# Kernel tuning notes

Measured on AMD Instinct MI355X. Metric: run time of the kernel, lower is better.

Reference implementation:

```python
import jax, jax.numpy as jnp
import numpy as np
import math

N_BITS = 8
NUM_GROUPS = 32
NUM_HEADS = 8
EPS = 1e-5


def fake_quant(x):
    # UniformAffineQuantizer: dynamic per-tensor asymmetric 8-bit fake quant
    levels = 2 ** N_BITS - 1
    xmin = jnp.minimum(x.min(), 0.0)
    xmax = jnp.maximum(x.max(), 0.0)
    scale = jnp.maximum((xmax - xmin) / levels, 1e-8)
    zp = jnp.round(-xmin / scale)
    xq = jnp.clip(jnp.round(x / scale) + zp, 0, levels)
    return (xq - zp) * scale


def group_norm(x, w, b):
    # x: (B, C, T)
    B, C, T = x.shape
    xg = x.reshape(B, NUM_GROUPS, C // NUM_GROUPS, T)
    mean = xg.mean(axis=(2, 3), keepdims=True)
    var = xg.var(axis=(2, 3), keepdims=True)
    xg = (xg - mean) * jax.lax.rsqrt(var + EPS)
    return xg.reshape(B, C, T) * w[None, :, None] + b[None, :, None]


def setup_inputs() -> dict:
    key = jax.random.key(0)
    ks = jax.random.split(key, 7)
    C = 512
    x = jax.random.normal(ks[0], (8, C, 32, 32), dtype=jnp.float32)
    gn_w = jnp.ones((C,), jnp.float32)
    gn_b = jnp.zeros((C,), jnp.float32)
    qkv_w = jax.random.normal(ks[1], (3 * C, C), jnp.float32) * (1.0 / math.sqrt(C))
    qkv_b = jax.random.normal(ks[2], (3 * C,), jnp.float32) * 0.01
    proj_w = jax.random.normal(ks[3], (C, C), jnp.float32) * (1.0 / math.sqrt(C))
    proj_b = jax.random.normal(ks[4], (C,), jnp.float32) * 0.01
    return {"x": x, "gn_w": gn_w, "gn_b": gn_b, "qkv_w": qkv_w,
            "qkv_b": qkv_b, "proj_w": proj_w, "proj_b": proj_b}


def reference(x, gn_w, gn_b, qkv_w, qkv_b, proj_w, proj_b):
    b, c, *spatial = x.shape
    T = int(np.prod(spatial))
    xf = x.reshape(b, c, T)                       # (B, C, T)
    h = group_norm(xf, gn_w, gn_b)
    qkv = jnp.einsum('oc,bct->bot', qkv_w, h) + qkv_b[None, :, None]  # (B, 3C, T)
    qkv = qkv.reshape(b * NUM_HEADS, -1, T)       # (B*H, 3*ch, T)
    ch = qkv.shape[1] // 3
    q, k, v = jnp.split(qkv, 3, axis=1)
    q = fake_quant(q)
    k = fake_quant(k)
    v = fake_quant(v)
    scale = 1.0 / math.sqrt(math.sqrt(ch))
    w = jnp.einsum('bct,bcs->bts', q * scale, k * scale)
    w = jax.nn.softmax(w.astype(jnp.float32), axis=-1).astype(q.dtype)
    a = jnp.einsum('bts,bcs->bct', w, v)          # (B*H, ch, T)
    a = a.reshape(b, c, T)
    a = jnp.einsum('oc,bct->bot', proj_w, a) + proj_b[None, :, None]
    return (xf + a).reshape(b, c, *spatial)
```

## Files before the change

kernel.cpp:

```cpp
#include <hip/hip_runtime.h>

typedef __attribute__((ext_vector_type(8))) __bf16 bf16x8;
typedef __attribute__((ext_vector_type(4))) __bf16 bf16x4;
typedef __attribute__((ext_vector_type(4))) float  f32x4;


static constexpr size_t QKV_OFF = 0;
static constexpr size_t HT_OFF  = 50331648;
static constexpr size_t WQ_OFF  = HT_OFF + 8388608;
static constexpr size_t WP_OFF  = WQ_OFF + 1572864;
static constexpr size_t MM_OFF  = WP_OFF + 524288;
static constexpr size_t KI_OFF  = MM_OFF + 8192;
static constexpr size_t VI_OFF  = KI_OFF + 8388608;
static constexpr size_t NEED_NEW = VI_OFF + 8388608;

__device__ __forceinline__ float dqi(float x, float inv_s, float zp) {
    float y = rintf(x * inv_s);
    return fminf(fmaxf(y, -zp), 255.0f - zp);
}
__device__ __forceinline__ f32x4 mfma16(bf16x8 a, bf16x8 b, f32x4 c) {
    return __builtin_amdgcn_mfma_f32_16x16x32_bf16(a, b, c, 0, 0, 0);
}
__device__ __forceinline__ float exp2i(float x) {
    float r;
    asm("v_exp_f32 %0, %1" : "=v"(r) : "v"(x));
    return r;
}
__device__ __forceinline__ void glds16(const __bf16* g, __bf16* l) {
    __builtin_amdgcn_global_load_lds((const __attribute__((address_space(1))) void*)g,
                                     (__attribute__((address_space(3))) void*)l, 16, 0, 0);
}
template <int N> __device__ __forceinline__ void waitv() {
    asm volatile("s_waitcnt vmcnt(%0)" :: "n"(N) : "memory");
}
__device__ __forceinline__ void bar_raw() {
    asm volatile("s_barrier" ::: "memory");
}

__device__ __forceinline__ void red_mm(const float* __restrict__ pmm, int id, int tid,
                                       float* sred, float& mn_out, float& mx_out) {
    float mn = pmm[id * 512 + tid * 2];
    float mx = pmm[id * 512 + tid * 2 + 1];
#pragma unroll
    for (int m = 1; m < 64; m <<= 1) {
        mn = fminf(mn, __shfl_xor(mn, m));
        mx = fmaxf(mx, __shfl_xor(mx, m));
    }
    if ((tid & 63) == 0) { sred[(tid >> 6) * 2] = mn; sred[(tid >> 6) * 2 + 1] = mx; }
    __syncthreads();
    mn = fminf(fminf(sred[0], sred[2]), fminf(sred[4], sred[6]));
    mx = fmaxf(fmaxf(sred[1], sred[3]), fmaxf(sred[5], sred[7]));
    __syncthreads();
    mn_out = fminf(mn, 0.0f);
    mx_out = fmaxf(mx, 0.0f);
}

__device__ __forceinline__ void red_mm8(const float* __restrict__ pmm, int id, int tid,
                                        float* sred, float& mn_out, float& mx_out) {
    int slot = tid & 255;
    float mn = pmm[id * 512 + slot * 2];
    float mx = pmm[id * 512 + slot * 2 + 1];
#pragma unroll
    for (int m = 1; m < 64; m <<= 1) {
        mn = fminf(mn, __shfl_xor(mn, m));
        mx = fmaxf(mx, __shfl_xor(mx, m));
    }
    if ((tid & 63) == 0) { sred[(tid >> 6) * 2] = mn; sred[(tid >> 6) * 2 + 1] = mx; }
    __syncthreads();
    float a = fminf(fminf(sred[0], sred[2]), fminf(sred[4], sred[6]));
    float b = fminf(fminf(sred[8], sred[10]), fminf(sred[12], sred[14]));
    mn = fminf(a, b);
    a = fmaxf(fmaxf(sred[1], sred[3]), fmaxf(sred[5], sred[7]));
    b = fmaxf(fmaxf(sred[9], sred[11]), fmaxf(sred[13], sred[15]));
    mx = fmaxf(a, b);
    __syncthreads();
    mn_out = fminf(mn, 0.0f);
    mx_out = fmaxf(mx, 0.0f);
}

__global__ __launch_bounds__(256) void gnprep(const float* __restrict__ x,
                                              const float* __restrict__ w,
                                              const float* __restrict__ bv,
                                              __bf16* __restrict__ hT,
                                              const float* __restrict__ qw,
                                              __bf16* __restrict__ wq,
                                              const float* __restrict__ pw,
                                              __bf16* __restrict__ wp) {
    int bid = blockIdx.x, tid = threadIdx.x;
    if (bid < 1024) {
        if (bid < 768) {
            int i = bid * 256 + tid;
            float4 v = ((const float4*)qw)[i];
            bf16x4 o = {(__bf16)v.x, (__bf16)v.y, (__bf16)v.z, (__bf16)v.w};
            ((bf16x4*)wq)[i] = o;
        } else {
            int i = (bid - 768) * 256 + tid;
            float4 v = ((const float4*)pw)[i];
            bf16x4 o = {(__bf16)v.x, (__bf16)v.y, (__bf16)v.z, (__bf16)v.w};
            ((bf16x4*)wp)[i] = o;
        }
        return;
    }
    int blk = bid - 1024;
    int b = blk >> 5, g = blk & 31;
    const float* xp = x + (size_t)(b * 512 + g * 16) * 1024;

    float4 v[16];
    float sum = 0.f, ss = 0.f;
#pragma unroll
    for (int i = 0; i < 16; ++i) {
        v[i] = *(const float4*)(xp + (size_t)i * 1024 + tid * 4);
        sum += v[i].x + v[i].y + v[i].z + v[i].w;
        ss  += v[i].x * v[i].x + v[i].y * v[i].y + v[i].z * v[i].z + v[i].w * v[i].w;
    }
#pragma unroll
    for (int m = 1; m < 64; m <<= 1) {
        sum += __shfl_xor(sum, m);
        ss  += __shfl_xor(ss, m);
    }
    __shared__ float s1[4], s2[4];
    int wid = tid >> 6;
    if ((tid & 63) == 0) { s1[wid] = sum; s2[wid] = ss; }
    __syncthreads();
    sum = s1[0] + s1[1] + s1[2] + s1[3];
    ss  = s2[0] + s2[1] + s2[2] + s2[3];
    float mean = sum * (1.0f / 16384.0f);
    float var  = ss * (1.0f / 16384.0f) - mean * mean;
    float rstd = rsqrtf(var + 1e-5f);

    float wc[16], bc[16];
#pragma unroll
    for (int c = 0; c < 16; ++c) { wc[c] = w[g * 16 + c] * rstd; bc[c] = bv[g * 16 + c]; }

#pragma unroll
    for (int j = 0; j < 4; ++j) {
        int t = tid * 4 + j;
        bf16x8 o0, o1;
#pragma unroll
        for (int c = 0; c < 8; ++c)
            o0[c] = (__bf16)(((&v[c].x)[j] - mean) * wc[c] + bc[c]);
#pragma unroll
        for (int c = 0; c < 8; ++c)
            o1[c] = (__bf16)(((&v[c + 8].x)[j] - mean) * wc[c + 8] + bc[c + 8]);
        __bf16* hp = hT + ((size_t)b * 1024 + t) * 512 + g * 16;
        *(bf16x8*)hp = o0;
        *(bf16x8*)(hp + 8) = o1;
    }
}

template <int MTILE, int MOT, bool MINMAX, bool RESID>
__global__ __launch_bounds__(256, 2) void mgemm5(const __bf16* __restrict__ A,
                                                 const __bf16* __restrict__ Bt,
                                                 const float* __restrict__ bias,
                                                 const float* __restrict__ resid,
                                                 float* __restrict__ out,
                                                 int M, float* __restrict__ pmm) {
    constexpr int NF  = (MTILE == 128) ? 4 : 2;
    constexpr int ASZ = MTILE * 64;
    constexpr int BSZ = 128 * 64;
    constexpr int LA  = MTILE / 32;
    constexpr int L   = LA + 4;
    constexpr int STG = 2 * (ASZ + BSZ) * 2;
    constexpr int CSB = 64 * 132 * 4;
    __shared__ __attribute__((aligned(16))) char smem_raw[(STG > CSB) ? STG : CSB];
    __bf16* sA0 = (__bf16*)smem_raw;
    __bf16* sA1 = sA0 + ASZ;
    __bf16* sB0 = sA1 + ASZ;
    __bf16* sB1 = sB0 + BSZ;
    __shared__ float smn[4], smx[4];

    int tid = threadIdx.x;
    int l = tid & 63, w = tid >> 6;
    int lo = l & 15, hi = l >> 4;

    int f = blockIdx.x;
    constexpr int NWG = MOT * 64;
    int wg = (f & 7) * (NWG / 8) + (f >> 3);
    int mo = wg % MOT, nb = wg / MOT;
    int nt = nb & 7, b = nb >> 3;

    const __bf16* Ap = A + (size_t)mo * MTILE * 512;
    const __bf16* Bp = Bt + ((size_t)b * 1024 + (size_t)nt * 128) * 512;
    int m0 = (MTILE == 128) ? (w >> 1) * 64 : 0;
    int n0 = (MTILE == 128) ? (w & 1) * 64 : w * 32;
    f32x4 acc[4][NF] = {};
    int scd = tid & 7;

    auto STAGE = [&](__bf16* dA, __bf16* dB, int k0) {
#pragma unroll
        for (int p = 0; p < LA; ++p) {
            int lin = p * 2048 + tid * 8;
            int row = lin >> 6;
            glds16(Ap + (size_t)row * 512 + k0 + ((scd ^ (row & 7)) << 3), dA + lin);
        }
#pragma unroll
        for (int p = 0; p < 4; ++p) {
            int lin = p * 2048 + tid * 8;
            int row = lin >> 6;
            glds16(Bp + (size_t)row * 512 + k0 + ((scd ^ (row & 7)) << 3), dB + lin);
        }
    };
    auto COMPUTE = [&](const __bf16* cA, const __bf16* cB) {
#pragma unroll
        for (int kk = 0; kk < 2; ++kk) {
            int rch = ((kk * 4 + hi) ^ (lo & 7)) << 3;
            bf16x8 af[4], bfr[NF];
#pragma unroll
            for (int i = 0; i < 4; ++i) af[i] = *(const bf16x8*)&cA[(m0 + 16 * i + lo) * 64 + rch];
#pragma unroll
            for (int j = 0; j < NF; ++j) bfr[j] = *(const bf16x8*)&cB[(n0 + 16 * j + lo) * 64 + rch];
#pragma unroll
            for (int i = 0; i < 4; ++i)
#pragma unroll
                for (int j = 0; j < NF; ++j) acc[i][j] = mfma16(af[i], bfr[j], acc[i][j]);
        }
    };

    STAGE(sA0, sB0, 0);
#pragma unroll
    for (int kp = 0; kp < 8; kp += 2) {
        if (kp + 1 < 8) { STAGE(sA1, sB1, (kp + 1) * 64); waitv<L>(); } else { waitv<0>(); }
        bar_raw();
        COMPUTE(sA0, sB0);
        bar_raw();
        if (kp + 2 < 8) { STAGE(sA0, sB0, (kp + 2) * 64); waitv<L>(); } else { waitv<0>(); }
        bar_raw();
        COMPUTE(sA1, sB1);
        bar_raw();
    }

    float* cs = (float*)smem_raw;
    float mn = 1e30f, mx = -1e30f;
    constexpr int NH = (MTILE == 128) ? 2 : 1;
#pragma unroll
    for (int h = 0; h < NH; ++h) {
        __syncthreads();
        if (MTILE == 64 || (w >> 1) == h) {
#pragma unroll
            for (int i = 0; i < 4; ++i)
#pragma unroll
                for (int r = 0; r < 4; ++r) {
                    int rl = 16 * i + hi * 4 + r;
                    float bi = bias[mo * MTILE + h * 64 + rl];
#pragma unroll
                    for (int j = 0; j < NF; ++j)
                        cs[rl * 132 + n0 + 16 * j + lo] = acc[i][j][r] + bi;
                }
        }
        __syncthreads();
#pragma unroll
        for (int it = 0; it < 8; ++it) {
            int lin = it * 256 + tid;
            int rr = lin >> 5, cc = (lin & 31) << 2;
            float4 v = *(const float4*)&cs[rr * 132 + cc];
            if (MINMAX) {
                mn = fminf(mn, fminf(fminf(v.x, v.y), fminf(v.z, v.w)));
                mx = fmaxf(mx, fmaxf(fmaxf(v.x, v.y), fmaxf(v.z, v.w)));
            }
            int grow = mo * MTILE + h * 64 + rr;
            size_t gaddr = ((size_t)b * M + grow) * 1024 + nt * 128 + cc;
            if (RESID) {
                float4 rv = *(const float4*)&resid[gaddr];
                v.x += rv.x; v.y += rv.y; v.z += rv.z; v.w += rv.w;
            }
            *(float4*)&out[gaddr] = v;
        }
    }

    if (MINMAX) {
#pragma unroll
        for (int msk = 1; msk < 64; msk <<= 1) {
            mn = fminf(mn, __shfl_xor(mn, msk));
            mx = fmaxf(mx, __shfl_xor(mx, msk));
        }
        if (l == 0) { smn[w] = mn; smx[w] = mx; }
        __syncthreads();
        if (tid == 0) {
            mn = fminf(fminf(smn[0], smn[1]), fminf(smn[2], smn[3]));
            mx = fmaxf(fmaxf(smx[0], smx[1]), fmaxf(smx[2], smx[3]));
            int id = mo >> 2;
            int slot = nb * 4 + (mo & 3);
            pmm[id * 512 + slot * 2]     = mn;
            pmm[id * 512 + slot * 2 + 1] = mx;
        }
    }
}

__global__ __launch_bounds__(256) void quant_kv(const float* __restrict__ qkv,
                                                const float* __restrict__ pmm,
                                                __bf16* __restrict__ ki,
                                                __bf16* __restrict__ vi) {
    int bh = blockIdx.x, tt = blockIdx.y;
    int b = bh >> 3, hh = bh & 7;
    int t0 = tt * 64;
    const float* kg = qkv + ((size_t)(b * 1536 + hh * 192) + 64) * 1024;
    const float* vg = kg + 65536;
    int tid = threadIdx.x;

    __shared__ float sred[8];
    float mn1, mx1, mn2, mx2;
    red_mm(pmm, 1, tid, sred, mn1, mx1);
    red_mm(pmm, 2, tid, sred, mn2, mx2);
    float ksc = fmaxf((mx1 - mn1) * (1.f / 255.f), 1e-8f), kzp = rintf(-mn1 / ksc);
    float vsc = fmaxf((mx2 - mn2) * (1.f / 255.f), 1e-8f), vzp = rintf(-mn2 / vsc);
    float inv_k = 1.f / ksc, inv_v = 1.f / vsc;

    __shared__ __bf16 sT[64][68];
    int cr = tid >> 4, t4 = tid & 15;
    int s = tid >> 2, c0 = (tid & 3) * 16;

    __bf16* vd = vi + (size_t)bh * 65536;
#pragma unroll
    for (int r = 0; r < 4; ++r) {
        int c = 16 * r + cr;
        float4 v = *(const float4*)(vg + (size_t)c * 1024 + t0 + t4 * 4);
        bf16x4 o = {(__bf16)dqi(v.x, inv_v, vzp), (__bf16)dqi(v.y, inv_v, vzp),
                    (__bf16)dqi(v.z, inv_v, vzp), (__bf16)dqi(v.w, inv_v, vzp)};
        *(bf16x4*)(vd + (size_t)c * 1024 + t0 + t4 * 4) = o;
    }

#pragma unroll
    for (int r = 0; r < 4; ++r) {
        int c = 16 * r + cr;
        float4 v = *(const float4*)(kg + (size_t)c * 1024 + t0 + t4 * 4);
        sT[t4 * 4 + 0][c] = (__bf16)dqi(v.x, inv_k, kzp);
        sT[t4 * 4 + 1][c] = (__bf16)dqi(v.y, inv_k, kzp);
        sT[t4 * 4 + 2][c] = (__bf16)dqi(v.z, inv_k, kzp);
        sT[t4 * 4 + 3][c] = (__bf16)dqi(v.w, inv_k, kzp);
    }
    __syncthreads();
    bf16x8 a0 = *(const bf16x8*)&sT[s][c0];
    bf16x8 a1 = *(const bf16x8*)&sT[s][c0 + 8];
    __bf16* kd = ki + ((size_t)bh * 1024 + t0 + s) * 64 + c0;
    *(bf16x8*)kd = a0;
    *(bf16x8*)(kd + 8) = a1;
}

__global__ __launch_bounds__(512, 4) void attn5(const float* __restrict__ qkv,
                                                const __bf16* __restrict__ ki,
                                                const __bf16* __restrict__ vi,
                                                const float* __restrict__ pmm,
                                                __bf16* __restrict__ aT) {
    int f = blockIdx.x;
    int bh = (f & 7) * 8 + ((f >> 3) & 7);
    int tt = f >> 6;
    int b = bh >> 3, hh = bh & 7;
    int t0 = tt * 128;
    const float* qg = qkv + (size_t)(b * 1536 + hh * 192) * 1024;
    const __bf16* kb = ki + (size_t)bh * 65536;
    const __bf16* vb = vi + (size_t)bh * 65536;
    int tid = threadIdx.x;

    __shared__ float sred[16];
    float mn0, mx0, mn1, mx1, mn2, mx2;
    red_mm8(pmm, 0, tid, sred, mn0, mx0);
    red_mm8(pmm, 1, tid, sred, mn1, mx1);
    red_mm8(pmm, 2, tid, sred, mn2, mx2);
    float qsc = fmaxf((mx0 - mn0) * (1.f / 255.f), 1e-8f), qzp = rintf(-mn0 / qsc);
    float ksc = fmaxf((mx1 - mn1) * (1.f / 255.f), 1e-8f);
    float vsc = fmaxf((mx2 - mn2) * (1.f / 255.f), 1e-8f);
    float inv_q = 1.f / qsc;
    float alpha2 = qsc * ksc * 0.125f * 1.4426950408889634f;
    float thr = 11.5415603f / alpha2;

    __shared__ __bf16 sh[128][72];
    __shared__ __bf16 kS[2][4096];
    __shared__ __bf16 vS[2][4096];
    int l = tid & 63, w = tid >> 6;
    int lo = l & 15, hi = l >> 4;

    int srow = tid >> 3, sc = tid & 7;
    int swz = (sc ^ (srow & 7)) << 3;
    const __bf16* kROW = kb + (size_t)srow * 64;
    const __bf16* vROW = vb + (size_t)srow * 1024;
    int lx = lo & 7;
    int rc0 = (hi ^ lx) << 3;
    int rc1 = ((4 + hi) ^ lx) << 3;

    bf16x8 kr = *(const bf16x8*)(kROW + sc * 8);
    bf16x8 vr = *(const bf16x8*)(vROW + sc * 8);

    {
        int c0 = (tid >> 5) * 4;
        int tl = tid & 31;
#pragma unroll
        for (int r = 0; r < 4; ++r) {
            int t = tl + 32 * r;
            float y0 = dqi(qg[(size_t)(c0 + 0) * 1024 + t0 + t], inv_q, qzp);
            float y1 = dqi(qg[(size_t)(c0 + 1) * 1024 + t0 + t], inv_q, qzp);
            float y2 = dqi(qg[(size_t)(c0 + 2) * 1024 + t0 + t], inv_q, qzp);
            float y3 = dqi(qg[(size_t)(c0 + 3) * 1024 + t0 + t], inv_q, qzp);
            bf16x4 o = {(__bf16)y0, (__bf16)y1, (__bf16)y2, (__bf16)y3};
            *(bf16x4*)&sh[t][c0] = o;
        }
    }
    __syncthreads();
    bf16x8 qf0 = *(const bf16x8*)&sh[16 * w + lo][hi * 8];
    bf16x8 qf1 = *(const bf16x8*)&sh[16 * w + lo][32 + hi * 8];
    *(bf16x8*)(kS[0] + srow * 64 + swz) = kr;
    *(bf16x8*)(vS[0] + srow * 64 + swz) = vr;
    __syncthreads();

    f32x4 acc0 = {}, acc1 = {}, acc2 = {}, acc3 = {};
    float m_run = -1e30f, l_run = 0.f;

    for (int st = 0; st < 16; ++st) {
        const __bf16* kc = kS[st & 1];
        const __bf16* vc = vS[st & 1];
        if (st < 15) {
            kr = *(const bf16x8*)(kROW + (st + 1) * 4096 + sc * 8);
            vr = *(const bf16x8*)(vROW + (st + 1) * 64 + sc * 8);
        }

        f32x4 sf[4] = {};
        __builtin_amdgcn_s_setprio(1);
#pragma unroll
        for (int sm = 0; sm < 4; ++sm)
            sf[sm] = mfma16(*(const bf16x8*)(kc + (16 * sm + lo) * 64 + rc0), qf0, sf[sm]);
#pragma unroll
        for (int sm = 0; sm < 4; ++sm)
            sf[sm] = mfma16(*(const bf16x8*)(kc + (16 * sm + lo) * 64 + rc1), qf1, sf[sm]);
        __builtin_amdgcn_s_setprio(0);

        float tm = -1e30f;
#pragma unroll
        for (int sm = 0; sm < 4; ++sm) {
            float a = fmaxf(sf[sm][0], sf[sm][1]);
            float c = fmaxf(sf[sm][2], sf[sm][3]);
            tm = fmaxf(tm, fmaxf(a, c));
        }
        tm = fmaxf(tm, __shfl_xor(tm, 16));
        tm = fmaxf(tm, __shfl_xor(tm, 32));
        if (!__all(tm <= m_run + thr)) {
            float mnew = fmaxf(m_run, tm);
            float fr = exp2i(alpha2 * (m_run - mnew));
            acc0 *= fr; acc1 *= fr; acc2 *= fr; acc3 *= fr;
            l_run *= fr;
            m_run = mnew;
        }
        float cc = -alpha2 * m_run;
        float ts = 0.f;
#pragma unroll
        for (int sm = 0; sm < 4; ++sm)
#pragma unroll
            for (int r = 0; r < 4; ++r) {
                float p = exp2i(fmaf(sf[sm][r], alpha2, cc));
                sf[sm][r] = p;
                ts += p;
            }
        ts += __shfl_xor(ts, 16);
        ts += __shfl_xor(ts, 32);
        l_run += ts;

#pragma unroll
        for (int sm = 0; sm < 4; ++sm) {
            bf16x4 pb = {(__bf16)sf[sm][0], (__bf16)sf[sm][1], (__bf16)sf[sm][2], (__bf16)sf[sm][3]};
            *(bf16x4*)&sh[16 * w + lo][16 * sm + hi * 4] = pb;
        }
        bf16x8 pf0 = *(const bf16x8*)&sh[16 * w + lo][hi * 8];
        bf16x8 pf1 = *(const bf16x8*)&sh[16 * w + lo][32 + hi * 8];

        __builtin_amdgcn_s_setprio(1);
        acc0 = mfma16(*(const bf16x8*)(vc + (lo) * 64 + rc0), pf0, acc0);
        acc1 = mfma16(*(const bf16x8*)(vc + (16 + lo) * 64 + rc0), pf0, acc1);
        acc2 = mfma16(*(const bf16x8*)(vc + (32 + lo) * 64 + rc0), pf0, acc2);
        acc3 = mfma16(*(const bf16x8*)(vc + (48 + lo) * 64 + rc0), pf0, acc3);
        acc0 = mfma16(*(const bf16x8*)(vc + (lo) * 64 + rc1), pf1, acc0);
        acc1 = mfma16(*(const bf16x8*)(vc + (16 + lo) * 64 + rc1), pf1, acc1);
        acc2 = mfma16(*(const bf16x8*)(vc + (32 + lo) * 64 + rc1), pf1, acc2);
        acc3 = mfma16(*(const bf16x8*)(vc + (48 + lo) * 64 + rc1), pf1, acc3);
        __builtin_amdgcn_s_setprio(0);

        if (st < 15) {
            *(bf16x8*)(kS[(st + 1) & 1] + srow * 64 + swz) = kr;
            *(bf16x8*)(vS[(st + 1) & 1] + srow * 64 + swz) = vr;
        }
        __syncthreads();
    }

    float rl = vsc / l_run;
    {
        bf16x4 o0 = {(__bf16)(acc0[0] * rl), (__bf16)(acc0[1] * rl), (__bf16)(acc0[2] * rl), (__bf16)(acc0[3] * rl)};
        bf16x4 o1 = {(__bf16)(acc1[0] * rl), (__bf16)(acc1[1] * rl), (__bf16)(acc1[2] * rl), (__bf16)(acc1[3] * rl)};
        bf16x4 o2 = {(__bf16)(acc2[0] * rl), (__bf16)(acc2[1] * rl), (__bf16)(acc2[2] * rl), (__bf16)(acc2[3] * rl)};
        bf16x4 o3 = {(__bf16)(acc3[0] * rl), (__bf16)(acc3[1] * rl), (__bf16)(acc3[2] * rl), (__bf16)(acc3[3] * rl)};
        *(bf16x4*)&sh[16 * w + lo][0  + hi * 4] = o0;
        *(bf16x4*)&sh[16 * w + lo][16 + hi * 4] = o1;
        *(bf16x4*)&sh[16 * w + lo][32 + hi * 4] = o2;
        *(bf16x4*)&sh[16 * w + lo][48 + hi * 4] = o3;
    }
    __syncthreads();
    __bf16* ap = aT + ((size_t)b * 1024 + t0 + (tid >> 2)) * 512 + hh * 64;
    bf16x8 v0 = *(const bf16x8*)&sh[tid >> 2][(tid & 3) * 8];
    bf16x8 v1 = *(const bf16x8*)&sh[tid >> 2][32 + (tid & 3) * 8];
    *(bf16x8*)(ap + (tid & 3) * 8) = v0;
    *(bf16x8*)(ap + 32 + (tid & 3) * 8) = v1;
}

__global__ __launch_bounds__(256) void attn_mfma(const float* __restrict__ qkv,
                                                 const float* __restrict__ pmm,
                                                 __bf16* __restrict__ aT) {
    int f = blockIdx.x;
    int bh = (f & 7) * 8 + ((f >> 3) & 7);
    int tt = f >> 6;
    int b = bh >> 3, hh = bh & 7;
    int t0 = tt * 64;
    const float* qg = qkv + (size_t)(b * 1536 + hh * 192) * 1024;
    const float* kg = qg + (size_t)64 * 1024;
    const float* vg = qg + (size_t)128 * 1024;
    int tid = threadIdx.x;

    __shared__ float sred[8];
    float mn0, mx0, mn1, mx1, mn2, mx2;
    red_mm(pmm, 0, tid, sred, mn0, mx0);
    red_mm(pmm, 1, tid, sred, mn1, mx1);
    red_mm(pmm, 2, tid, sred, mn2, mx2);
    float qsc = fmaxf((mx0 - mn0) * (1.f / 255.f), 1e-8f), qzp = rintf(-mn0 / qsc);
    float ksc = fmaxf((mx1 - mn1) * (1.f / 255.f), 1e-8f), kzp = rintf(-mn1 / ksc);
    float vsc = fmaxf((mx2 - mn2) * (1.f / 255.f), 1e-8f), vzp = rintf(-mn2 / vsc);
    float inv_q = 1.f / qsc, inv_k = 1.f / ksc, inv_v = 1.f / vsc;
    float alpha = qsc * ksc * 0.125f;

    __shared__ __bf16 qT[64][72];
    __shared__ __bf16 kT[64][72];
    __shared__ __bf16 vL[64][72];
    __shared__ __bf16 pL[4][16][72];

    int l = tid & 63, w = tid >> 6;
    int lo = l & 15, hi = l >> 4;
    int c0 = (tid >> 4) * 4;
    int tl = tid & 15;

#pragma unroll
    for (int r = 0; r < 4; ++r) {
        int t = tl + 16 * r;
        float y0 = dqi(qg[(size_t)(c0 + 0) * 1024 + t0 + t], inv_q, qzp);
        float y1 = dqi(qg[(size_t)(c0 + 1) * 1024 + t0 + t], inv_q, qzp);
        float y2 = dqi(qg[(size_t)(c0 + 2) * 1024 + t0 + t], inv_q, qzp);
        float y3 = dqi(qg[(size_t)(c0 + 3) * 1024 + t0 + t], inv_q, qzp);
        bf16x4 o = {(__bf16)y0, (__bf16)y1, (__bf16)y2, (__bf16)y3};
        *(bf16x4*)&qT[t][c0] = o;
    }
    __syncthreads();
    bf16x8 qf0 = *(const bf16x8*)&qT[16 * w + lo][hi * 8];
    bf16x8 qf1 = *(const bf16x8*)&qT[16 * w + lo][32 + hi * 8];

    f32x4 acc0 = {}, acc1 = {}, acc2 = {}, acc3 = {};
    float m_run = -1e30f, l_run = 0.f;

    for (int st = 0; st < 16; ++st) {
        int s0 = st * 64;
        __syncthreads();
#pragma unroll
        for (int r = 0; r < 4; ++r) {
            int srow = tl + 16 * r;
            float y0 = dqi(kg[(size_t)(c0 + 0) * 1024 + s0 + srow], inv_k, kzp);
            float y1 = dqi(kg[(size_t)(c0 + 1) * 1024 + s0 + srow], inv_k, kzp);
            float y2 = dqi(kg[(size_t)(c0 + 2) * 1024 + s0 + srow], inv_k, kzp);
            float y3 = dqi(kg[(size_t)(c0 + 3) * 1024 + s0 + srow], inv_k, kzp);
            bf16x4 ok = {(__bf16)y0, (__bf16)y1, (__bf16)y2, (__bf16)y3};
            *(bf16x4*)&kT[srow][c0] = ok;
            int c = (tid >> 4) + 16 * r;
            float4 vv = *(const float4*)(vg + (size_t)c * 1024 + s0 + (tid & 15) * 4);
            bf16x4 ov = {(__bf16)dqi(vv.x, inv_v, vzp), (__bf16)dqi(vv.y, inv_v, vzp),
                         (__bf16)dqi(vv.z, inv_v, vzp), (__bf16)dqi(vv.w, inv_v, vzp)};
            *(bf16x4*)&vL[c][(tid & 15) * 4] = ov;
        }
        __syncthreads();

        f32x4 sf[4] = {};
#pragma unroll
        for (int sm = 0; sm < 4; ++sm)
            sf[sm] = mfma16(*(const bf16x8*)&kT[16 * sm + lo][hi * 8], qf0, sf[sm]);
#pragma unroll
        for (int sm = 0; sm < 4; ++sm)
            sf[sm] = mfma16(*(const bf16x8*)&kT[16 * sm + lo][32 + hi * 8], qf1, sf[sm]);

        float tm = -1e30f;
#pragma unroll
        for (int sm = 0; sm < 4; ++sm)
#pragma unroll
            for (int r = 0; r < 4; ++r) { sf[sm][r] *= alpha; tm = fmaxf(tm, sf[sm][r]); }
        tm = fmaxf(tm, __shfl_xor(tm, 16));
        tm = fmaxf(tm, __shfl_xor(tm, 32));
        float mnew = fmaxf(m_run, tm);
        float ts = 0.f;
#pragma unroll
        for (int sm = 0; sm < 4; ++sm)
#pragma unroll
            for (int r = 0; r < 4; ++r) {
                float p = __expf(sf[sm][r] - mnew);
                sf[sm][r] = p;
                ts += p;
            }
        ts += __shfl_xor(ts, 16);
        ts += __shfl_xor(ts, 32);
        float fr = __expf(m_run - mnew);
        l_run = l_run * fr + ts;
        m_run = mnew;
        acc0 *= fr; acc1 *= fr; acc2 *= fr; acc3 *= fr;

#pragma unroll
        for (int sm = 0; sm < 4; ++sm) {
            bf16x4 pb = {(__bf16)sf[sm][0], (__bf16)sf[sm][1], (__bf16)sf[sm][2], (__bf16)sf[sm][3]};
            *(bf16x4*)&pL[w][lo][16 * sm + hi * 4] = pb;
        }
        bf16x8 pf0 = *(const bf16x8*)&pL[w][lo][hi * 8];
        bf16x8 pf1 = *(const bf16x8*)&pL[w][lo][32 + hi * 8];
        acc0 = mfma16(*(const bf16x8*)&vL[lo][hi * 8], pf0, acc0);
        acc1 = mfma16(*(const bf16x8*)&vL[16 + lo][hi * 8], pf0, acc1);
        acc2 = mfma16(*(const bf16x8*)&vL[32 + lo][hi * 8], pf0, acc2);
        acc3 = mfma16(*(const bf16x8*)&vL[48 + lo][hi * 8], pf0, acc3);
        acc0 = mfma16(*(const bf16x8*)&vL[lo][32 + hi * 8], pf1, acc0);
        acc1 = mfma16(*(const bf16x8*)&vL[16 + lo][32 + hi * 8], pf1, acc1);
        acc2 = mfma16(*(const bf16x8*)&vL[32 + lo][32 + hi * 8], pf1, acc2);
        acc3 = mfma16(*(const bf16x8*)&vL[48 + lo][32 + hi * 8], pf1, acc3);
    }

    float rl = vsc / l_run;
    __syncthreads();
    {
        bf16x4 o0 = {(__bf16)(acc0[0] * rl), (__bf16)(acc0[1] * rl), (__bf16)(acc0[2] * rl), (__bf16)(acc0[3] * rl)};
        bf16x4 o1 = {(__bf16)(acc1[0] * rl), (__bf16)(acc1[1] * rl), (__bf16)(acc1[2] * rl), (__bf16)(acc1[3] * rl)};
        bf16x4 o2 = {(__bf16)(acc2[0] * rl), (__bf16)(acc2[1] * rl), (__bf16)(acc2[2] * rl), (__bf16)(acc2[3] * rl)};
        bf16x4 o3 = {(__bf16)(acc3[0] * rl), (__bf16)(acc3[1] * rl), (__bf16)(acc3[2] * rl), (__bf16)(acc3[3] * rl)};
        *(bf16x4*)&qT[16 * w + lo][0  + hi * 4] = o0;
        *(bf16x4*)&qT[16 * w + lo][16 + hi * 4] = o1;
        *(bf16x4*)&qT[16 * w + lo][32 + hi * 4] = o2;
        *(bf16x4*)&qT[16 * w + lo][48 + hi * 4] = o3;
    }
    __syncthreads();
    __bf16* ap = aT + ((size_t)b * 1024 + t0 + (tid >> 2)) * 512 + hh * 64;
    bf16x8 v0 = *(const bf16x8*)&qT[tid >> 2][(tid & 3) * 8];
    bf16x8 v1 = *(const bf16x8*)&qT[tid >> 2][32 + (tid & 3) * 8];
    *(bf16x8*)(ap + (tid & 3) * 8) = v0;
    *(bf16x8*)(ap + 32 + (tid & 3) * 8) = v1;
}

extern "C" void kernel_launch(void* const* d_in, const int* in_sizes, int n_in,
                              void* d_out, int out_size, void* d_ws, size_t ws_size,
                              hipStream_t stream) {
    const float* x      = (const float*)d_in[0];
    const float* gn_w   = (const float*)d_in[1];
    const float* gn_b   = (const float*)d_in[2];
    const float* qkv_w  = (const float*)d_in[3];
    const float* qkv_b  = (const float*)d_in[4];
    const float* proj_w = (const float*)d_in[5];
    const float* proj_b = (const float*)d_in[6];
    char* ws = (char*)d_ws;
    float*    qkv = (float*)(ws + QKV_OFF);
    __bf16*   hT  = (__bf16*)(ws + HT_OFF);
    __bf16*   wq  = (__bf16*)(ws + WQ_OFF);
    __bf16*   wp  = (__bf16*)(ws + WP_OFF);
    float*    pmm = (float*)(ws + MM_OFF);
    __bf16*   ki  = (__bf16*)(ws + KI_OFF);
    __bf16*   vi  = (__bf16*)(ws + VI_OFF);
    float* out = (float*)d_out;

    gnprep<<<1280, 256, 0, stream>>>(x, gn_w, gn_b, hT, qkv_w, wq, proj_w, wp);
    mgemm5<128, 12, true, false><<<768, 256, 0, stream>>>(wq, hT, qkv_b, nullptr, qkv, 1536, pmm);
    if (ws_size >= NEED_NEW) {
        quant_kv<<<dim3(64, 16), 256, 0, stream>>>(qkv, pmm, ki, vi);
        attn5<<<512, 512, 0, stream>>>(qkv, ki, vi, pmm, hT);
    } else {
        attn_mfma<<<1024, 256, 0, stream>>>(qkv, pmm, hT);
    }
    mgemm5<64, 8, false, true><<<512, 256, 0, stream>>>(wp, hT, proj_b, x, out, 512, nullptr);
}
```

Measured before the change: 92.64 us.

## Split group norm into stats and apply kernels with coalesced transposed writes

The fused group-norm kernel wrote hT with 16-byte scattered stores per token. It is now split into a stats kernel that writes per-group mean and rstd to workspace, and an apply kernel that transposes through LDS so each row of hT is written with coalesced stores. This adds an extra launch and a second read of x. The quant_kv grid is also flattened so batch is the fastest-varying index, which changes block scheduling order.

```diff
diff --git a/kernel.cpp b/kernel.cpp
--- a/kernel.cpp
+++ b/kernel.cpp
@@ -10,6 +10,7 @@
 static constexpr size_t WQ_OFF  = HT_OFF + 8388608;
 static constexpr size_t WP_OFF  = WQ_OFF + 1572864;
 static constexpr size_t MM_OFF  = WP_OFF + 524288;
+static constexpr size_t GST_OFF = MM_OFF + 6144;
 static constexpr size_t KI_OFF  = MM_OFF + 8192;
 static constexpr size_t VI_OFF  = KI_OFF + 8388608;
 static constexpr size_t NEED_NEW = VI_OFF + 8388608;
@@ -78,14 +79,12 @@
     mx_out = fmaxf(mx, 0.0f);
 }
 
-__global__ __launch_bounds__(256) void gnprep(const float* __restrict__ x,
-                                              const float* __restrict__ w,
-                                              const float* __restrict__ bv,
-                                              __bf16* __restrict__ hT,
-                                              const float* __restrict__ qw,
-                                              __bf16* __restrict__ wq,
-                                              const float* __restrict__ pw,
-                                              __bf16* __restrict__ wp) {
+__global__ __launch_bounds__(256) void gnstats(const float* __restrict__ x,
+                                               const float* __restrict__ qw,
+                                               __bf16* __restrict__ wq,
+                                               const float* __restrict__ pw,
+                                               __bf16* __restrict__ wp,
+                                               float* __restrict__ gst) {
     int bid = blockIdx.x, tid = threadIdx.x;
     if (bid < 1024) {
         if (bid < 768) {
@@ -105,13 +104,12 @@
     int b = blk >> 5, g = blk & 31;
     const float* xp = x + (size_t)(b * 512 + g * 16) * 1024;
 
-    float4 v[16];
     float sum = 0.f, ss = 0.f;
 #pragma unroll
     for (int i = 0; i < 16; ++i) {
-        v[i] = *(const float4*)(xp + (size_t)i * 1024 + tid * 4);
-        sum += v[i].x + v[i].y + v[i].z + v[i].w;
-        ss  += v[i].x * v[i].x + v[i].y * v[i].y + v[i].z * v[i].z + v[i].w * v[i].w;
+        float4 v = *(const float4*)(xp + (size_t)i * 1024 + tid * 4);
+        sum += v.x + v.y + v.z + v.w;
+        ss  += v.x * v.x + v.y * v.y + v.z * v.z + v.w * v.w;
     }
 #pragma unroll
     for (int m = 1; m < 64; m <<= 1) {
@@ -122,29 +120,50 @@
     int wid = tid >> 6;
     if ((tid & 63) == 0) { s1[wid] = sum; s2[wid] = ss; }
     __syncthreads();
-    sum = s1[0] + s1[1] + s1[2] + s1[3];
-    ss  = s2[0] + s2[1] + s2[2] + s2[3];
-    float mean = sum * (1.0f / 16384.0f);
-    float var  = ss * (1.0f / 16384.0f) - mean * mean;
-    float rstd = rsqrtf(var + 1e-5f);
-
-    float wc[16], bc[16];
-#pragma unroll
-    for (int c = 0; c < 16; ++c) { wc[c] = w[g * 16 + c] * rstd; bc[c] = bv[g * 16 + c]; }
-
-#pragma unroll
-    for (int j = 0; j < 4; ++j) {
-        int t = tid * 4 + j;
-        bf16x8 o0, o1;
-#pragma unroll
-        for (int c = 0; c < 8; ++c)
-            o0[c] = (__bf16)(((&v[c].x)[j] - mean) * wc[c] + bc[c]);
-#pragma unroll
-        for (int c = 0; c < 8; ++c)
-            o1[c] = (__bf16)(((&v[c + 8].x)[j] - mean) * wc[c + 8] + bc[c + 8]);
-        __bf16* hp = hT + ((size_t)b * 1024 + t) * 512 + g * 16;
-        *(bf16x8*)hp = o0;
-        *(bf16x8*)(hp + 8) = o1;
+    if (tid == 0) {
+        sum = s1[0] + s1[1] + s1[2] + s1[3];
+        ss  = s2[0] + s2[1] + s2[2] + s2[3];
+        float mean = sum * (1.0f / 16384.0f);
+        float var  = ss * (1.0f / 16384.0f) - mean * mean;
+        gst[blk]       = mean;
+        gst[256 + blk] = rsqrtf(var + 1e-5f);
+    }
+}
+
+__global__ __launch_bounds__(256) void gnapply(const float* __restrict__ x,
+                                               const float* __restrict__ w,
+                                               const float* __restrict__ bv,
+                                               const float* __restrict__ gst,
+                                               __bf16* __restrict__ hT) {
+    int f = blockIdx.x;
+    int b = f & 7, ts = f >> 3;
+    int t0 = ts * 32;
+    int tid = threadIdx.x;
+
+    __shared__ __bf16 sH[32][520];
+    int cl = tid >> 3;
+    int tl = (tid & 7) * 4;
+
+#pragma unroll
+    for (int ci = 0; ci < 16; ++ci) {
+        int c = ci * 32 + cl;
+        int g = c >> 4;
+        float mean = gst[b * 32 + g];
+        float rstd = gst[256 + b * 32 + g];
+        float wc = w[c] * rstd, bc = bv[c];
+        float4 v = *(const float4*)(x + ((size_t)(b * 512 + c)) * 1024 + t0 + tl);
+        sH[tl + 0][c] = (__bf16)((v.x - mean) * wc + bc);
+        sH[tl + 1][c] = (__bf16)((v.y - mean) * wc + bc);
+        sH[tl + 2][c] = (__bf16)((v.z - mean) * wc + bc);
+        sH[tl + 3][c] = (__bf16)((v.w - mean) * wc + bc);
+    }
+    __syncthreads();
+    int lane = tid & 63, wv = tid >> 6;
+#pragma unroll
+    for (int it = 0; it < 8; ++it) {
+        int row = it * 4 + wv;
+        bf16x8 o = *(const bf16x8*)&sH[row][lane * 8];
+        *(bf16x8*)(hT + ((size_t)(b * 1024 + t0 + row)) * 512 + lane * 8) = o;
     }
 }
 
@@ -290,8 +309,11 @@
                                                 const float* __restrict__ pmm,
                                                 __bf16* __restrict__ ki,
                                                 __bf16* __restrict__ vi) {
-    int bh = blockIdx.x, tt = blockIdx.y;
-    int b = bh >> 3, hh = bh & 7;
+    int f = blockIdx.x;
+    int b = f & 7;
+    int r2 = f >> 3;
+    int hh = r2 & 7, tt = r2 >> 3;
+    int bh = b * 8 + hh;
     int t0 = tt * 64;
     const float* kg = qkv + ((size_t)(b * 1536 + hh * 192) + 64) * 1024;
     const float* vg = kg + 65536;
@@ -653,14 +675,16 @@
     __bf16*   wq  = (__bf16*)(ws + WQ_OFF);
     __bf16*   wp  = (__bf16*)(ws + WP_OFF);
     float*    pmm = (float*)(ws + MM_OFF);
+    float*    gst = (float*)(ws + GST_OFF);
     __bf16*   ki  = (__bf16*)(ws + KI_OFF);
     __bf16*   vi  = (__bf16*)(ws + VI_OFF);
     float* out = (float*)d_out;
 
-    gnprep<<<1280, 256, 0, stream>>>(x, gn_w, gn_b, hT, qkv_w, wq, proj_w, wp);
+    gnstats<<<1280, 256, 0, stream>>>(x, qkv_w, wq, proj_w, wp, gst);
+    gnapply<<<256, 256, 0, stream>>>(x, gn_w, gn_b, gst, hT);
     mgemm5<128, 12, true, false><<<768, 256, 0, stream>>>(wq, hT, qkv_b, nullptr, qkv, 1536, pmm);
     if (ws_size >= NEED_NEW) {
-        quant_kv<<<dim3(64, 16), 256, 0, stream>>>(qkv, pmm, ki, vi);
+        quant_kv<<<1024, 256, 0, stream>>>(qkv, pmm, ki, vi);
         attn5<<<512, 512, 0, stream>>>(qkv, ki, vi, pmm, hT);
     } else {
         attn_mfma<<<1024, 256, 0, stream>>>(qkv, pmm, hT);
```

New measurement: 93.91 us (median of 3 runs). No clear change (+1.4%).
